# Optimization experiments

Hardware: AMD Instinct MI355X
Metric: run time of the kernel (lower is better)

## Reference

```python
import jax, jax.numpy as jnp
import numpy as np

CHUNK = 32
H = 4

def silu(x):
    return x * jax.nn.sigmoid(x)

def l2norm(x):
    return x * jax.lax.rsqrt(jnp.sum(x * x, -1, keepdims=True) + 1e-6)

def dwconv_causal(x_cl, w):
    # x_cl: (b, C, L), w: (C, k) depthwise causal conv (cross-correlation, left pad k-1)
    k = w.shape[1]
    xp = jnp.pad(x_cl, ((0, 0), (0, 0), (k - 1, 0)))
    return jax.lax.conv_general_dilated(xp, w[:, None, :], (1,), 'VALID',
        dimension_numbers=('NCH', 'OIH', 'NCH'), feature_group_count=x_cl.shape[1])

def short_conv_silu(x_bld, w):
    y = dwconv_causal(jnp.swapaxes(x_bld, 1, 2), w)
    return silu(jnp.swapaxes(y, 1, 2))

def delta_rule_chunkwise(q, k, v, beta, chunk=CHUNK):
    # q,k: (b,h,L,dk)  v: (b,h,L,dv)  beta: (b,h,L)
    b, h, L, dk = q.shape
    dv = v.shape[-1]
    pad = (-L) % chunk
    if pad:
        q, k, v = (jnp.pad(t, ((0, 0), (0, 0), (0, pad), (0, 0))) for t in (q, k, v))
        beta = jnp.pad(beta, ((0, 0), (0, 0), (0, pad)))
    n = (L + pad) // chunk
    q = l2norm(q)
    k = l2norm(k)
    v = v * beta[..., None]
    kb = k * beta[..., None]
    ch = lambda x: x.reshape(b, h, n, chunk, x.shape[-1])
    qc, kc, vc, kbc = map(ch, (q, k, v, kb))
    idx = jnp.arange(chunk)
    strict_lower = (idx[:, None] > idx[None, :]).astype(q.dtype)
    incl_lower = (idx[:, None] >= idx[None, :]).astype(q.dtype)
    # forward substitution to invert (I - tril(beta K K^T, -1)) per chunk
    attn = -jnp.einsum('bhncd,bhned->bhnce', kbc, kc) * strict_lower
    for i in range(1, chunk):
        upd = jnp.einsum('...j,...ji->...i', attn[..., i, :], attn[..., :, :i])
        attn = attn.at[..., i, :i].add(upd)
    attn = attn + jnp.eye(chunk, dtype=q.dtype)
    u = attn @ vc          # (b,h,n,c,dv)
    w = attn @ kbc         # (b,h,n,c,dk)
    xs = tuple(jnp.moveaxis(t, 2, 0) for t in (qc, kc, u, w))
    S0 = jnp.zeros((b, h, dk, dv), q.dtype)
    def step(S, x):
        qi, ki, ui, wi = x
        a_loc = jnp.einsum('bhcd,bhed->bhce', qi, ki) * incl_lower
        ui = ui - wi @ S
        oi = qi @ S + a_loc @ ui
        S = S + jnp.einsum('bhcd,bhcv->bhdv', ki, ui)
        return S, oi
    S, o = jax.lax.scan(step, S0, xs)
    o = jnp.moveaxis(o, 0, 2).reshape(b, h, n * chunk, dv)[:, :, :L]
    return o, S

def multiscale_conv(v, ms_w3, ms_w15, ms_w31, kernel_mix_w, channel_mixer_w):
    # v: (b,l,h,d)
    b, l, h, d = v.shape
    x = jnp.swapaxes(v.reshape(b, l, h * d), 1, 2)  # (b, h*d, l)
    outs = [dwconv_causal(x, w) for w in (ms_w3, ms_w15, ms_w31)]
    y = jnp.concatenate(outs, axis=1)               # (b, 3*h*d, l)
    # faithful to torch rearrange 'b (h kd) l -> b l h kd' on the concat layout
    y = y.reshape(b, h, 3 * d, l).transpose(0, 3, 1, 2)  # (b,l,h,3d)
    y = y @ kernel_mix_w                            # (b,l,h,d)
    y = (y.reshape(b, l, h * d) @ channel_mixer_w).reshape(b, l, h, d)
    return y

def _forward(hidden_states, Wq, Wk, Wv, Wb, conv_q_w, conv_k_w, conv_v_w,
             ms_w3, ms_w15, ms_w31, kernel_mix_w, channel_mixer_w,
             fusion_w1, fusion_b1, fusion_w2, fusion_b2, o_norm_w, Wo):
    b, L, D = hidden_states.shape
    h = H
    dk = Wq.shape[1] // h
    dv = Wv.shape[1] // h
    q = short_conv_silu(hidden_states @ Wq, conv_q_w).reshape(b, L, h, dk)
    k = short_conv_silu(hidden_states @ Wk, conv_k_w).reshape(b, L, h, dk)
    v = short_conv_silu(hidden_states @ Wv, conv_v_w).reshape(b, L, h, dv)
    v_direct = v
    beta = jax.nn.sigmoid(hidden_states @ Wb)  # (b,L,h)
    tr = lambda x: jnp.swapaxes(x, 1, 2)
    delta_out, _S = delta_rule_chunkwise(tr(q), tr(k), tr(v), tr(beta))
    delta_out = jnp.swapaxes(delta_out, 1, 2)  # (b,L,h,dv)
    ms_out = multiscale_conv(v_direct, ms_w3, ms_w15, ms_w31, kernel_mix_w, channel_mixer_w)
    bn = lambda x: jnp.mean(jnp.abs(x), -1)    # (b,L,h)
    gate_features = jnp.concatenate([hidden_states, bn(ms_out), bn(delta_out), bn(v_direct)], -1)
    hdn = jax.nn.gelu(gate_features @ fusion_w1 + fusion_b1, approximate=False)
    logits = (hdn @ fusion_w2 + fusion_b2).reshape(b, L, h, 3)
    wts = jax.nn.softmax(logits, -1)
    o = wts[..., 0:1] * ms_out + wts[..., 1:2] * delta_out + wts[..., 2:3] * v_direct
    o = o * jax.lax.rsqrt(jnp.mean(o * o, -1, keepdims=True) + 1e-5) * o_norm_w  # RMSNorm
    return o.reshape(b, L, h * dv) @ Wo

def setup_inputs() -> dict:
    B, L, D = 4, 2048, 1024
    h, d = H, D // H
    key = jax.random.key(0)
    ks = jax.random.split(key, 20)
    nrm = lambda k, shp, s: (jax.random.normal(k, shp, dtype=jnp.float32) * s)
    inp = {
        'hidden_states': nrm(ks[0], (B, L, D), 1.0),
        'Wq': nrm(ks[1], (D, D), D ** -0.5),
        'Wk': nrm(ks[2], (D, D), D ** -0.5),
        'Wv': nrm(ks[3], (D, D), D ** -0.5),
        'Wb': nrm(ks[4], (D, h), D ** -0.5),
        'conv_q_w': nrm(ks[5], (D, 4), 0.3),
        'conv_k_w': nrm(ks[6], (D, 4), 0.3),
        'conv_v_w': nrm(ks[7], (D, 4), 0.3),
        'ms_w3': nrm(ks[8], (D, 3), 0.02),
        'ms_w15': nrm(ks[9], (D, 15), 0.02),
        'ms_w31': nrm(ks[10], (D, 31), 0.02),
        'kernel_mix_w': nrm(ks[11], (3 * d, d), (3 * d) ** -0.5),
        'channel_mixer_w': nrm(ks[12], (D, D), D ** -0.5),
        'fusion_w1': nrm(ks[13], (D + 3 * h, 2 * D), (D + 3 * h) ** -0.5),
        'fusion_b1': jnp.zeros((2 * D,), jnp.float32),
        'fusion_w2': nrm(ks[14], (2 * D, 3 * h), (2 * D) ** -0.5),
        'fusion_b2': jnp.concatenate([jnp.zeros((2 * h,), jnp.float32), jnp.ones((h,), jnp.float32)]),
        'o_norm_w': jnp.ones((d,), jnp.float32),
        'Wo': nrm(ks[15], (D, D), D ** -0.5),
    }
    return inp

def reference(hidden_states, Wq, Wk, Wv, Wb, conv_q_w, conv_k_w, conv_v_w,
              ms_w3, ms_w15, ms_w31, kernel_mix_w, channel_mixer_w,
              fusion_w1, fusion_b1, fusion_w2, fusion_b2, o_norm_w, Wo):
    return _forward(hidden_states, Wq, Wk, Wv, Wb, conv_q_w, conv_k_w, conv_v_w,
                    ms_w3, ms_w15, ms_w31, kernel_mix_w, channel_mixer_w,
                    fusion_w1, fusion_b1, fusion_w2, fusion_b2, o_norm_w, Wo)
```

## Files before the change

kernel.cpp:

```cpp
#include <hip/hip_runtime.h>
#include <math.h>


typedef __attribute__((ext_vector_type(8))) __bf16 bf16x8;
typedef __attribute__((ext_vector_type(4))) float f32x4;

__device__ inline ushort f2bf(float f) {
    union { float f; unsigned u; } x; x.f = f;
    unsigned u = x.u;
    u += 0x7fffu + ((u >> 16) & 1u);
    return (ushort)(u >> 16);
}
__device__ inline float bf2f(ushort h) {
    union { unsigned u; float f; } x; x.u = ((unsigned)h) << 16;
    return x.f;
}
__device__ inline float ldf(float v) { return v; }
__device__ inline float ldf(ushort v) { return bf2f(v); }

template<int EPI>
__global__ __launch_bounds__(256) void gemm_mfma(
    const ushort* __restrict__ A, const ushort* __restrict__ BT,
    const float* __restrict__ bias, const float* __restrict__ extA,
    const float* __restrict__ extB, void* __restrict__ Cout,
    int M, int N, int K)
{
    __shared__ ushort As[128 * 32];
    __shared__ ushort Bs[128 * 32];
    __shared__ float bns[(EPI >= 2) ? 128 * 13 : 1];
    __shared__ float exb[(EPI >= 2) ? 12 * 128 : 1];
    const int tid = threadIdx.x;
    const int row0 = blockIdx.y * 128, col0 = blockIdx.x * 128;
    const int lane = tid & 63, wave = tid >> 6;
    const int wr = (wave >> 1) * 64, wc = (wave & 1) * 64;

    if (EPI >= 2) {
        for (int e = tid; e < 128 * 12; e += 256)
            bns[(e / 12) * 13 + (e % 12)] = extA[(long)(row0 + e / 12) * 12 + e % 12];
        for (int e = tid; e < 12 * 128; e += 256)
            exb[e] = extB[(long)(e >> 7) * N + col0 + (e & 127)];
    }

    f32x4 acc[4][4];
    #pragma unroll
    for (int m = 0; m < 4; ++m)
        #pragma unroll
        for (int n = 0; n < 4; ++n) {
            acc[m][n][0] = 0.f; acc[m][n][1] = 0.f;
            acc[m][n][2] = 0.f; acc[m][n][3] = 0.f;
        }

    const int rA = lane & 15;
    const int ko = (lane >> 4) * 8;
    const int srow = tid >> 2;
    const int skk = (tid & 3) * 8;

    for (int k0 = 0; k0 < K; k0 += 32) {
        #pragma unroll
        for (int i = 0; i < 2; ++i) {
            const long ga = (long)(row0 + i * 64 + srow) * K + k0 + skk;
            __builtin_amdgcn_global_load_lds(
                (const __attribute__((address_space(1))) void*)(A + ga),
                (__attribute__((address_space(3))) void*)(As + i * 2048 + wave * 512),
                16, 0, 0);
            const long gb = (long)(col0 + i * 64 + srow) * K + k0 + skk;
            __builtin_amdgcn_global_load_lds(
                (const __attribute__((address_space(1))) void*)(BT + gb),
                (__attribute__((address_space(3))) void*)(Bs + i * 2048 + wave * 512),
                16, 0, 0);
        }
        __syncthreads();
        bf16x8 af[4], bfr[4];
        #pragma unroll
        for (int m = 0; m < 4; ++m)
            af[m] = *(const bf16x8*)(As + (wr + m * 16 + rA) * 32 + ko);
        #pragma unroll
        for (int n = 0; n < 4; ++n)
            bfr[n] = *(const bf16x8*)(Bs + (wc + n * 16 + rA) * 32 + ko);
        #pragma unroll
        for (int m = 0; m < 4; ++m)
            #pragma unroll
            for (int n = 0; n < 4; ++n)
                acc[m][n] = __builtin_amdgcn_mfma_f32_16x16x32_bf16(af[m], bfr[n], acc[m][n], 0, 0, 0);
        __syncthreads();
    }

    const int crow = (lane >> 4) * 4;
    const int ccol = lane & 15;
    #pragma unroll
    for (int m = 0; m < 4; ++m) {
        #pragma unroll
        for (int n = 0; n < 4; ++n) {
            #pragma unroll
            for (int r = 0; r < 4; ++r) {
                const int rl = wr + m * 16 + crow + r;
                const int cl = wc + n * 16 + ccol;
                float vv = acc[m][n][r];
                if (EPI >= 2) {
                    vv += bias[col0 + cl];
                    #pragma unroll
                    for (int j = 0; j < 12; ++j) vv += bns[rl * 13 + j] * exb[j * 128 + cl];
                    vv = 0.5f * vv * (1.f + erff(vv * 0.70710678118654752f));
                }
                const long off = (long)(row0 + rl) * N + col0 + cl;
                if (EPI == 0) ((float*)Cout)[off] = vv;
                else ((ushort*)Cout)[off] = f2bf(vv);
            }
        }
    }
}

__global__ __launch_bounds__(256) void transpose_cast(const float* __restrict__ W,
    ushort* __restrict__ WT, int K, int N)
{
    __shared__ float t[32][33];
    const int k0 = blockIdx.y * 32, n0 = blockIdx.x * 32;
    const int c = threadIdx.x & 31, r8 = threadIdx.x >> 5;
    #pragma unroll
    for (int rr = 0; rr < 4; ++rr) {
        const int r = r8 + rr * 8;
        t[r][c] = W[(long)(k0 + r) * N + n0 + c];
    }
    __syncthreads();
    #pragma unroll
    for (int rr = 0; rr < 4; ++rr) {
        const int r = r8 + rr * 8;
        WT[(long)(n0 + r) * K + k0 + c] = f2bf(t[c][r]);
    }
}

__global__ __launch_bounds__(256) void cast_bf16(const float* __restrict__ x,
    ushort* __restrict__ y)
{
    const long i = ((long)blockIdx.x * 256 + threadIdx.x) * 4;
    const float4 v = *(const float4*)(x + i);
    ushort4 o;
    o.x = f2bf(v.x); o.y = f2bf(v.y); o.z = f2bf(v.z); o.w = f2bf(v.w);
    *(ushort4*)(y + i) = o;
}

template<int NOUT, int MODE, typename TA>
__global__ __launch_bounds__(256) void gemm_smallN(const TA* __restrict__ A,
    const float* __restrict__ Bm, const float* __restrict__ bias,
    float* __restrict__ Cm, int K)
{
    __shared__ float part[4][NOUT];
    __shared__ float sm[NOUT];
    const int m = blockIdx.x, tid = threadIdx.x;
    const TA* ar = A + (long)m * K;
    float acc[NOUT];
    #pragma unroll
    for (int j = 0; j < NOUT; ++j) acc[j] = 0.f;
    for (int k = tid; k < K; k += 256) {
        const float a = ldf(ar[k]);
        #pragma unroll
        for (int j = 0; j < NOUT; ++j) acc[j] += a * Bm[(long)k * NOUT + j];
    }
    #pragma unroll
    for (int j = 0; j < NOUT; ++j)
        for (int off = 32; off > 0; off >>= 1) acc[j] += __shfl_down(acc[j], off);
    const int wid = tid >> 6, lane = tid & 63;
    if (lane == 0) {
        #pragma unroll
        for (int j = 0; j < NOUT; ++j) part[wid][j] = acc[j];
    }
    __syncthreads();
    if (tid < NOUT) {
        float s = part[0][tid] + part[1][tid] + part[2][tid] + part[3][tid];
        if (MODE == 0) {
            Cm[(long)m * NOUT + tid] = 1.f / (1.f + expf(-s));
        } else {
            sm[tid] = s + bias[tid];
        }
    }
    if (MODE == 1) {
        __syncthreads();
        if (tid < NOUT) {
            const int hh = tid / 3, r = tid - hh * 3;
            const float a0 = sm[hh * 3], a1 = sm[hh * 3 + 1], a2 = sm[hh * 3 + 2];
            const float mx = fmaxf(a0, fmaxf(a1, a2));
            const float e0 = expf(a0 - mx), e1 = expf(a1 - mx), e2 = expf(a2 - mx);
            const float mine = (r == 0) ? e0 : ((r == 1) ? e1 : e2);
            Cm[(long)m * NOUT + tid] = mine / (e0 + e1 + e2);
        }
    }
}

__global__ __launch_bounds__(256) void conv4_silu(const float* __restrict__ x,
    const float* __restrict__ wc, float* __restrict__ y)
{
    const long idx = (long)blockIdx.x * 256 + threadIdx.x;
    const int c = (int)(idx & 1023);
    const long bl = idx >> 10;
    const int l = (int)(bl & 2047);
    const long b = bl >> 11;
    const float* xp = x + b * 2048 * 1024 + c;
    const float* wp = wc + c * 4;
    float s = 0.f;
    #pragma unroll
    for (int t = 0; t < 4; ++t) {
        const int ll = l - 3 + t;
        if (ll >= 0) s += xp[(long)ll * 1024] * wp[t];
    }
    y[idx] = s / (1.f + expf(-s));
}

__global__ __launch_bounds__(256) void l2norm_bf16(const float* __restrict__ x,
    ushort* __restrict__ y)
{
    const long wid = ((long)blockIdx.x * 256 + threadIdx.x) >> 6;
    const int lane = threadIdx.x & 63;
    const float4 xv = *(const float4*)(x + wid * 256 + lane * 4);
    float ss = xv.x * xv.x + xv.y * xv.y + xv.z * xv.z + xv.w * xv.w;
    for (int off = 32; off > 0; off >>= 1) ss += __shfl_down(ss, off);
    ss = __shfl(ss, 0);
    const float inv = rsqrtf(ss + 1e-6f);
    ushort4 o;
    o.x = f2bf(xv.x * inv); o.y = f2bf(xv.y * inv);
    o.z = f2bf(xv.z * inv); o.w = f2bf(xv.w * inv);
    *(ushort4*)(y + wid * 256 + lane * 4) = o;
}

__global__ __launch_bounds__(256) void chunk_prep(
    const ushort* __restrict__ qn, const ushort* __restrict__ kn,
    const float* __restrict__ v, const float* __restrict__ beta,
    float* __restrict__ u, ushort* __restrict__ w16,
    ushort* __restrict__ kT16, ushort* __restrict__ al16)
{
    __shared__ float kb_s[32 * 256];
    __shared__ float bufB[32 * 256];
    __shared__ float Ms[32 * 33];
    __shared__ float Rs[32 * 33];
    __shared__ float bet[32];
    const int blk = blockIdx.x;
    const int n = blk & 63;
    const int bh = blk >> 6;
    const int h = bh & 3;
    const int b = bh >> 2;
    const int tid = threadIdx.x;
    const long lbase = (long)b * 2048 + n * 32;

    if (tid < 32) bet[tid] = beta[(lbase + tid) * 4 + h];
    __syncthreads();
    for (int e = tid; e < 8192; e += 256) {
        const int c = e >> 8, dd = e & 255;
        const float kv = bf2f(kn[(lbase + c) * 1024 + h * 256 + dd]);
        bufB[dd * 32 + c] = kv;
        kb_s[c * 256 + dd] = kv * bet[c];
    }
    __syncthreads();
    for (int e = tid; e < 8192; e += 256)
        kT16[(long)blk * 8192 + e] = f2bf(bufB[e]);

    const int j = tid & 31, i0 = tid >> 5;
    {
        float m4[4] = {0.f, 0.f, 0.f, 0.f};
        for (int dd = 0; dd < 256; ++dd) {
            const float kt = bufB[dd * 32 + j];
            #pragma unroll
            for (int ii = 0; ii < 4; ++ii) m4[ii] += kb_s[(i0 + 8 * ii) * 256 + dd] * kt;
        }
        #pragma unroll
        for (int ii = 0; ii < 4; ++ii) {
            const int i = i0 + 8 * ii;
            const float mv = (i > j) ? -m4[ii] : 0.f;
            Ms[i * 33 + j] = mv;
            Rs[i * 33 + j] = mv + ((i == j) ? 1.f : 0.f);
        }
    }
    {
        float a4[4] = {0.f, 0.f, 0.f, 0.f};
        for (int dd = 0; dd < 256; ++dd) {
            const float kt = bufB[dd * 32 + j];
            #pragma unroll
            for (int ii = 0; ii < 4; ++ii)
                a4[ii] += bf2f(qn[(lbase + (i0 + 8 * ii)) * 1024 + h * 256 + dd]) * kt;
        }
        #pragma unroll
        for (int ii = 0; ii < 4; ++ii) {
            const int i = i0 + 8 * ii;
            al16[(long)blk * 1024 + i * 32 + j] = f2bf((i >= j) ? a4[ii] : 0.f);
        }
    }
    __syncthreads();
    for (int it = 0; it < 4; ++it) {
        float p4[4] = {0.f, 0.f, 0.f, 0.f};
        for (int kk = 0; kk < 32; ++kk) {
            const float pb = Ms[kk * 33 + j];
            #pragma unroll
            for (int ii = 0; ii < 4; ++ii) p4[ii] += Ms[(i0 + 8 * ii) * 33 + kk] * pb;
        }
        __syncthreads();
        #pragma unroll
        for (int ii = 0; ii < 4; ++ii) Ms[(i0 + 8 * ii) * 33 + j] = p4[ii];
        __syncthreads();
        float r4[4] = {0.f, 0.f, 0.f, 0.f};
        for (int kk = 0; kk < 32; ++kk) {
            const float pb = Ms[kk * 33 + j];
            #pragma unroll
            for (int ii = 0; ii < 4; ++ii) r4[ii] += Rs[(i0 + 8 * ii) * 33 + kk] * pb;
        }
        __syncthreads();
        #pragma unroll
        for (int ii = 0; ii < 4; ++ii) Rs[(i0 + 8 * ii) * 33 + j] += r4[ii];
        __syncthreads();
    }
    for (int e = tid; e < 8192; e += 256) {
        const int c = e >> 8, dd = e & 255;
        bufB[c * 256 + dd] = v[(lbase + c) * 1024 + h * 256 + dd] * bet[c];
    }
    __syncthreads();
    {
        const int dd = tid;
        float accU[32], accW[32];
        #pragma unroll
        for (int r = 0; r < 32; ++r) { accU[r] = 0.f; accW[r] = 0.f; }
        for (int kk = 0; kk < 32; ++kk) {
            const float vv = bufB[kk * 256 + dd];
            const float bb = kb_s[kk * 256 + dd];
            #pragma unroll
            for (int r = 0; r < 32; ++r) {
                const float rr = Rs[r * 33 + kk];
                accU[r] += rr * vv;
                accW[r] += rr * bb;
            }
        }
        const long base = (long)blk * 32;
        #pragma unroll
        for (int r = 0; r < 32; ++r) {
            u  [(base + r) * 256 + dd] = accU[r];
            w16[(base + r) * 256 + dd] = f2bf(accW[r]);
        }
    }
}

__global__ __launch_bounds__(64) void delta_scan_mfma(
    const ushort* __restrict__ q16, const ushort* __restrict__ kT16,
    const ushort* __restrict__ w16, const float* __restrict__ u,
    const ushort* __restrict__ al16, float* __restrict__ dt)
{
    __shared__ __align__(16) ushort Stg[2][25600];
    __shared__ __align__(16) ushort Sb[16 * 264];
    __shared__ __align__(16) ushort Ub[16 * 40];
    const int blk = blockIdx.x;
    const int bh = blk & 15;
    const int sl = blk >> 4;
    const int h = bh & 3;
    const int b = bh >> 2;
    const int v0 = sl * 16;
    const int lane = threadIdx.x;
    const int col = lane & 15;
    const int grp = lane >> 4;
    const int l5 = lane & 31;
    const int lh = lane >> 5;

    f32x4 S[16];
    #pragma unroll
    for (int t = 0; t < 16; ++t) { S[t][0] = 0.f; S[t][1] = 0.f; S[t][2] = 0.f; S[t][3] = 0.f; }
    for (int i = lane; i < 16 * 264; i += 64) Sb[i] = 0;

    const ushort* Wg = w16  + (long)bh * 64 * 8192;
    const ushort* Qg = q16  + ((long)b * 2048) * 1024 + h * 256;
    const ushort* Kg = kT16 + (long)bh * 64 * 8192;
    const ushort* Ag = al16 + (long)bh * 64 * 1024;
    const float*  Ug = u    + (long)bh * 64 * 8192 + grp * 1024 + v0 + col;
    float*        dp = dt   + ((long)b * 2048 + grp * 4) * 1024 + h * 256 + v0 + col;

    auto STAGE = [&](int n, int s) {
        ushort* dst = &Stg[s][0];
        const ushort* wsrc = Wg + (long)n * 8192;
        #pragma unroll
        for (int i = 0; i < 16; ++i) {
            const int row = 2 * i + lh;
            const int key = row & 7;
            __builtin_amdgcn_global_load_lds(
                (const __attribute__((address_space(1))) void*)(wsrc + row * 256 + ((l5 ^ key) << 3)),
                (__attribute__((address_space(3))) void*)(dst + i * 512), 16, 0, 0);
        }
        #pragma unroll
        for (int i = 0; i < 16; ++i) {
            const int row = 2 * i + lh;
            const int key = row & 7;
            __builtin_amdgcn_global_load_lds(
                (const __attribute__((address_space(1))) void*)(Qg + (long)(n * 32 + row) * 1024 + ((l5 ^ key) << 3)),
                (__attribute__((address_space(3))) void*)(dst + 8192 + i * 512), 16, 0, 0);
        }
        const ushort* ksrc = Kg + (long)n * 8192;
        #pragma unroll
        for (int i = 0; i < 16; ++i)
            __builtin_amdgcn_global_load_lds(
                (const __attribute__((address_space(1))) void*)(ksrc + i * 512 + lane * 8),
                (__attribute__((address_space(3))) void*)(dst + 16384 + i * 512), 16, 0, 0);
        const ushort* asrc = Ag + (long)n * 1024;
        #pragma unroll
        for (int i = 0; i < 2; ++i)
            __builtin_amdgcn_global_load_lds(
                (const __attribute__((address_space(1))) void*)(asrc + i * 512 + lane * 8),
                (__attribute__((address_space(3))) void*)(dst + 24576 + i * 512), 16, 0, 0);
    };

    const int xk = (col & 7) << 3;

    STAGE(0, 0);
    for (int n = 0; n < 64; ++n) {
        const int s = n & 1;
        asm volatile("s_waitcnt vmcnt(0)" ::: "memory");
        __builtin_amdgcn_sched_barrier(0);
        float upre[8];
        #pragma unroll
        for (int rt = 0; rt < 2; ++rt)
            #pragma unroll
            for (int r = 0; r < 4; ++r)
                upre[rt * 4 + r] = Ug[(long)n * 8192 + rt * 4096 + r * 256];
        __builtin_amdgcn_sched_barrier(0);
        if (n < 63) STAGE(n + 1, s ^ 1);
        const ushort* Sg = &Stg[s][0];

        bf16x8 sf[8];
        #pragma unroll
        for (int kb = 0; kb < 8; ++kb)
            sf[kb] = *(const bf16x8*)&Sb[col * 264 + kb * 32 + grp * 8];

        f32x4 up[2];
        #pragma unroll
        for (int rt = 0; rt < 2; ++rt) {
            f32x4 a; a[0] = 0.f; a[1] = 0.f; a[2] = 0.f; a[3] = 0.f;
            #pragma unroll
            for (int kb = 0; kb < 8; ++kb) {
                const int widx = ((rt * 16 + col) << 8) + (((kb << 5) + (grp << 3)) ^ xk);
                const bf16x8 wf = *(const bf16x8*)&Sg[widx];
                a = __builtin_amdgcn_mfma_f32_16x16x32_bf16(wf, sf[kb], a, 0, 0, 0);
            }
            #pragma unroll
            for (int r = 0; r < 4; ++r)
                up[rt][r] = upre[rt * 4 + r] - a[r];
        }
        #pragma unroll
        for (int rt = 0; rt < 2; ++rt) {
            ushort4 p;
            p.x = f2bf(up[rt][0]); p.y = f2bf(up[rt][1]);
            p.z = f2bf(up[rt][2]); p.w = f2bf(up[rt][3]);
            *(ushort4*)&Ub[col * 40 + rt * 16 + grp * 4] = p;
        }
        const bf16x8 uf = *(const bf16x8*)&Ub[col * 40 + grp * 8];

        #pragma unroll
        for (int rt = 0; rt < 2; ++rt) {
            f32x4 a; a[0] = 0.f; a[1] = 0.f; a[2] = 0.f; a[3] = 0.f;
            #pragma unroll
            for (int kb = 0; kb < 8; ++kb) {
                const int qidx = 8192 + ((rt * 16 + col) << 8) + (((kb << 5) + (grp << 3)) ^ xk);
                const bf16x8 qf = *(const bf16x8*)&Sg[qidx];
                a = __builtin_amdgcn_mfma_f32_16x16x32_bf16(qf, sf[kb], a, 0, 0, 0);
            }
            const bf16x8 alf = *(const bf16x8*)&Sg[24576 + rt * 512 + col * 32 + grp * 8];
            a = __builtin_amdgcn_mfma_f32_16x16x32_bf16(alf, uf, a, 0, 0, 0);
            #pragma unroll
            for (int r = 0; r < 4; ++r)
                dp[(long)n * 32768 + rt * 16384 + r * 1024] = a[r];
        }

        #pragma unroll
        for (int t = 0; t < 16; ++t) {
            const bf16x8 kf = *(const bf16x8*)&Sg[16384 + t * 512 + col * 32 + grp * 8];
            S[t] = __builtin_amdgcn_mfma_f32_16x16x32_bf16(kf, uf, S[t], 0, 0, 0);
        }

        #pragma unroll
        for (int t = 0; t < 16; ++t) {
            ushort4 p;
            p.x = f2bf(S[t][0]); p.y = f2bf(S[t][1]);
            p.z = f2bf(S[t][2]); p.w = f2bf(S[t][3]);
            *(ushort4*)&Sb[col * 264 + t * 16 + grp * 4] = p;
        }
    }
}

__global__ __launch_bounds__(256) void ms_conv(const float* __restrict__ v,
    const float* __restrict__ w3, const float* __restrict__ w15,
    const float* __restrict__ w31, ushort* __restrict__ y)
{
    const int bid = blockIdx.x;
    const int b = bid >> 10;
    const int oct = (bid >> 2) & 255;
    const int c = ((bid & 3) << 8) + threadIdx.x;
    const int l0 = oct << 3;
    const float* vb = v + ((long)b * 2048) * 1024 + c;
    ushort* yb = y + ((long)b * 2048) * 3072 + c;

    float win[38];
    #pragma unroll
    for (int t = 0; t < 38; ++t) {
        const int ll = l0 - 30 + t;
        win[t] = (ll >= 0) ? vb[(long)ll * 1024] : 0.f;
    }
    {
        float W[31];
        #pragma unroll
        for (int t = 0; t < 31; ++t) W[t] = w31[c * 31 + t];
        #pragma unroll
        for (int j = 0; j < 8; ++j) {
            float s = 0.f;
            #pragma unroll
            for (int t = 0; t < 31; ++t) s += win[j + t] * W[t];
            yb[(long)(l0 + j) * 3072 + 2048] = f2bf(s);
        }
    }
    {
        float W[15];
        #pragma unroll
        for (int t = 0; t < 15; ++t) W[t] = w15[c * 15 + t];
        #pragma unroll
        for (int j = 0; j < 8; ++j) {
            float s = 0.f;
            #pragma unroll
            for (int t = 0; t < 15; ++t) s += win[j + 16 + t] * W[t];
            yb[(long)(l0 + j) * 3072 + 1024] = f2bf(s);
        }
    }
    {
        float W[3];
        #pragma unroll
        for (int t = 0; t < 3; ++t) W[t] = w3[c * 3 + t];
        #pragma unroll
        for (int j = 0; j < 8; ++j) {
            float s = 0.f;
            #pragma unroll
            for (int t = 0; t < 3; ++t) s += win[j + 28 + t] * W[t];
            yb[(long)(l0 + j) * 3072] = f2bf(s);
        }
    }
}

__global__ __launch_bounds__(256) void build_bn(const float* __restrict__ ms,
    const float* __restrict__ dt, const float* __restrict__ v,
    float* __restrict__ bn)
{
    const int bl = blockIdx.x, tid = threadIdx.x;
    const long rb = (long)bl * 1024;
    const int wid = tid >> 6, lane = tid & 63;
    const long base = rb + wid * 256 + lane * 4;
    float* g = bn + (long)bl * 12;
    float4 a;
    float s;
    a = *(const float4*)(ms + base);
    s = fabsf(a.x) + fabsf(a.y) + fabsf(a.z) + fabsf(a.w);
    for (int off = 32; off > 0; off >>= 1) s += __shfl_down(s, off);
    if (lane == 0) g[wid] = s * (1.f / 256.f);
    a = *(const float4*)(dt + base);
    s = fabsf(a.x) + fabsf(a.y) + fabsf(a.z) + fabsf(a.w);
    for (int off = 32; off > 0; off >>= 1) s += __shfl_down(s, off);
    if (lane == 0) g[4 + wid] = s * (1.f / 256.f);
    a = *(const float4*)(v + base);
    s = fabsf(a.x) + fabsf(a.y) + fabsf(a.z) + fabsf(a.w);
    for (int off = 32; off > 0; off >>= 1) s += __shfl_down(s, off);
    if (lane == 0) g[8 + wid] = s * (1.f / 256.f);
}

__global__ __launch_bounds__(256) void blend_rms(const float* __restrict__ ms,
    const float* __restrict__ dt, const float* __restrict__ v,
    const float* __restrict__ wts, const float* __restrict__ onw,
    ushort* __restrict__ o)
{
    const int bl = blockIdx.x, tid = threadIdx.x;
    const int wid = tid >> 6, lane = tid & 63;
    const long base = (long)bl * 1024 + wid * 256 + lane * 4;
    const float* wr = wts + (long)bl * 12 + wid * 3;
    const float w0 = wr[0], w1 = wr[1], w2 = wr[2];
    const float4 m = *(const float4*)(ms + base);
    const float4 d = *(const float4*)(dt + base);
    const float4 x = *(const float4*)(v + base);
    float4 ov;
    ov.x = w0 * m.x + w1 * d.x + w2 * x.x;
    ov.y = w0 * m.y + w1 * d.y + w2 * x.y;
    ov.z = w0 * m.z + w1 * d.z + w2 * x.z;
    ov.w = w0 * m.w + w1 * d.w + w2 * x.w;
    float ss = ov.x * ov.x + ov.y * ov.y + ov.z * ov.z + ov.w * ov.w;
    for (int off = 32; off > 0; off >>= 1) ss += __shfl_down(ss, off);
    ss = __shfl(ss, 0);
    const float inv = rsqrtf(ss * (1.f / 256.f) + 1e-5f);
    const float4 nw = *(const float4*)(onw + lane * 4);
    ushort4 ob;
    ob.x = f2bf(ov.x * inv * nw.x); ob.y = f2bf(ov.y * inv * nw.y);
    ob.z = f2bf(ov.z * inv * nw.z); ob.w = f2bf(ov.w * inv * nw.w);
    *(ushort4*)(o + base) = ob;
}

extern "C" void kernel_launch(void* const* d_in, const int* in_sizes, int n_in,
                              void* d_out, int out_size, void* d_ws, size_t ws_size,
                              hipStream_t stream)
{
    (void)in_sizes; (void)n_in; (void)out_size; (void)ws_size;
    const float* hid   = (const float*)d_in[0];
    const float* Wq    = (const float*)d_in[1];
    const float* Wk    = (const float*)d_in[2];
    const float* Wv    = (const float*)d_in[3];
    const float* Wb    = (const float*)d_in[4];
    const float* cq    = (const float*)d_in[5];
    const float* ck    = (const float*)d_in[6];
    const float* cv    = (const float*)d_in[7];
    const float* w3    = (const float*)d_in[8];
    const float* w15   = (const float*)d_in[9];
    const float* w31   = (const float*)d_in[10];
    const float* kmix  = (const float*)d_in[11];
    const float* cmix  = (const float*)d_in[12];
    const float* fw1   = (const float*)d_in[13];
    const float* fb1   = (const float*)d_in[14];
    const float* fw2   = (const float*)d_in[15];
    const float* fb2   = (const float*)d_in[16];
    const float* onw   = (const float*)d_in[17];
    const float* Wo    = (const float*)d_in[18];
    float* out = (float*)d_out;

    const size_t MiB = 1024 * 1024;
    char* W = (char*)d_ws;
    float*  s0    = (float*)(W);
    char*   s1c   = W + 32 * MiB;
    float*  s1    = (float*)s1c;
    float*  s2    = (float*)(W + 64 * MiB);
    char*   s3    = W + 96 * MiB;
    float*  s4    = (float*)(W + 128 * MiB);
    ushort* hid16 = (ushort*)(W + 160 * MiB);
    ushort* WqT   = (ushort*)(W + 176 * MiB);
    ushort* WkT   = WqT   + 1024 * 1024;
    ushort* WvT   = WkT   + 1024 * 1024;
    ushort* cmixT = WvT   + 1024 * 1024;
    ushort* WoT   = cmixT + 1024 * 1024;
    ushort* fw1T  = WoT   + 1024 * 1024;
    ushort* kmixT = fw1T  + 2048 * 1024;
    float*  beta  = (float*)(W + 191 * MiB);
    ushort* al16  = (ushort*)(W + 191 * MiB + 128 * 1024);
    float*  bnf   = (float*)(W + 193 * MiB + 128 * 1024);
    float*  wts   = bnf + 98304;

    ushort* q16    = (ushort*)s3;
    ushort* k16    = (ushort*)(s3 + 16 * MiB);
    ushort* mix16  = q16;
    ushort* ofin16 = k16;
    ushort* yms16  = (ushort*)s0;
    ushort* hdn16  = (ushort*)s0;
    float*  qlin = s0; float* qtmp = s1;
    float*  u = s0;
    ushort* w16  = (ushort*)s1c;
    ushort* kT16 = (ushort*)(s1c + 16 * MiB);
    float*  dt = s2; float* v = s4; float* msout = s1;

    const dim3 T256(256);
    cast_bf16<<<8192, T256, 0, stream>>>(hid, hid16);
    transpose_cast<<<dim3(32, 32), T256, 0, stream>>>(Wq, WqT, 1024, 1024);
    transpose_cast<<<dim3(32, 32), T256, 0, stream>>>(Wk, WkT, 1024, 1024);
    transpose_cast<<<dim3(32, 32), T256, 0, stream>>>(Wv, WvT, 1024, 1024);
    transpose_cast<<<dim3(32, 32), T256, 0, stream>>>(cmix, cmixT, 1024, 1024);
    transpose_cast<<<dim3(32, 32), T256, 0, stream>>>(Wo, WoT, 1024, 1024);
    transpose_cast<<<dim3(64, 32), T256, 0, stream>>>(fw1, fw1T, 1024, 2048);
    transpose_cast<<<dim3(8, 24), T256, 0, stream>>>(kmix, kmixT, 768, 256);
    gemm_mfma<0><<<dim3(8, 64), T256, 0, stream>>>(hid16, WqT, nullptr, nullptr, nullptr, qlin, 8192, 1024, 1024);
    conv4_silu<<<32768, T256, 0, stream>>>(qlin, cq, qtmp);
    l2norm_bf16<<<8192, T256, 0, stream>>>(qtmp, q16);
    gemm_mfma<0><<<dim3(8, 64), T256, 0, stream>>>(hid16, WkT, nullptr, nullptr, nullptr, qlin, 8192, 1024, 1024);
    conv4_silu<<<32768, T256, 0, stream>>>(qlin, ck, qtmp);
    l2norm_bf16<<<8192, T256, 0, stream>>>(qtmp, k16);
    gemm_mfma<0><<<dim3(8, 64), T256, 0, stream>>>(hid16, WvT, nullptr, nullptr, nullptr, qlin, 8192, 1024, 1024);
    conv4_silu<<<32768, T256, 0, stream>>>(qlin, cv, v);
    gemm_smallN<4, 0><<<8192, T256, 0, stream>>>(hid, Wb, nullptr, beta, 1024);
    chunk_prep<<<1024, T256, 0, stream>>>(q16, k16, v, beta, u, w16, kT16, al16);
    delta_scan_mfma<<<256, dim3(64), 0, stream>>>(q16, kT16, w16, u, al16, dt);
    ms_conv<<<4096, T256, 0, stream>>>(v, w3, w15, w31, yms16);
    gemm_mfma<1><<<dim3(2, 256), T256, 0, stream>>>(yms16, kmixT, nullptr, nullptr, nullptr, mix16, 32768, 256, 768);
    gemm_mfma<0><<<dim3(8, 64), T256, 0, stream>>>(mix16, cmixT, nullptr, nullptr, nullptr, msout, 8192, 1024, 1024);
    build_bn<<<8192, T256, 0, stream>>>(msout, dt, v, bnf);
    gemm_mfma<3><<<dim3(16, 64), T256, 0, stream>>>(hid16, fw1T, fb1, bnf, fw1 + 1024L * 2048, hdn16, 8192, 2048, 1024);
    gemm_smallN<12, 1><<<8192, T256, 0, stream>>>(hdn16, fw2, fb2, wts, 2048);
    blend_rms<<<8192, T256, 0, stream>>>(msout, dt, v, wts, onw, ofin16);
    gemm_mfma<0><<<dim3(8, 64), T256, 0, stream>>>(ofin16, WoT, nullptr, nullptr, nullptr, out, 8192, 1024, 1024);
}
```

Before: 875.9 us.

## Share staged W/K/alpha tiles across four waves in the delta scan

```diff
diff --git a/kernel.cpp b/kernel.cpp
--- a/kernel.cpp
+++ b/kernel.cpp
@@ -334,21 +334,24 @@
     }
 }
 
-__global__ __launch_bounds__(64) void delta_scan_mfma(
+__global__ __launch_bounds__(256) void delta_scan_mfma(
     const ushort* __restrict__ q16, const ushort* __restrict__ kT16,
     const ushort* __restrict__ w16, const float* __restrict__ u,
     const ushort* __restrict__ al16, float* __restrict__ dt)
 {
-    __shared__ __align__(16) ushort Stg[2][25600];
-    __shared__ __align__(16) ushort Sb[16 * 264];
-    __shared__ __align__(16) ushort Ub[16 * 40];
+    __shared__ __align__(16) ushort Stg[2][17408];
+    __shared__ __align__(16) ushort Sb[4][16 * 264];
+    __shared__ __align__(16) ushort Ub[4][16 * 40];
     const int blk = blockIdx.x;
     const int bh = blk & 15;
-    const int sl = blk >> 4;
+    const int qtr = blk >> 4;
+    const int tid = threadIdx.x;
+    const int wv = tid >> 6;
+    const int lane = tid & 63;
+    const int sl = qtr * 4 + wv;
     const int h = bh & 3;
     const int b = bh >> 2;
     const int v0 = sl * 16;
-    const int lane = threadIdx.x;
     const int col = lane & 15;
     const int grp = lane >> 4;
     const int l5 = lane & 31;
@@ -357,46 +360,44 @@
     f32x4 S[16];
     #pragma unroll
     for (int t = 0; t < 16; ++t) { S[t][0] = 0.f; S[t][1] = 0.f; S[t][2] = 0.f; S[t][3] = 0.f; }
-    for (int i = lane; i < 16 * 264; i += 64) Sb[i] = 0;
+    for (int i = lane; i < 16 * 264; i += 64) Sb[wv][i] = 0;
 
     const ushort* Wg = w16  + (long)bh * 64 * 8192;
     const ushort* Qg = q16  + ((long)b * 2048) * 1024 + h * 256;
     const ushort* Kg = kT16 + (long)bh * 64 * 8192;
     const ushort* Ag = al16 + (long)bh * 64 * 1024;
     const float*  Ug = u    + (long)bh * 64 * 8192 + grp * 1024 + v0 + col;
+    const ushort* qp = Qg + col * 1024 + grp * 8;
     float*        dp = dt   + ((long)b * 2048 + grp * 4) * 1024 + h * 256 + v0 + col;
 
-    auto STAGE = [&](int n, int s) {
-        ushort* dst = &Stg[s][0];
+    auto STAGE = [&](int n, int sb) {
+        ushort* dst = &Stg[sb][0];
         const ushort* wsrc = Wg + (long)n * 8192;
         #pragma unroll
-        for (int i = 0; i < 16; ++i) {
-            const int row = 2 * i + lh;
+        for (int i = 0; i < 4; ++i) {
+            const int blkW = wv * 4 + i;
+            const int row = 2 * blkW + lh;
             const int key = row & 7;
             __builtin_amdgcn_global_load_lds(
                 (const __attribute__((address_space(1))) void*)(wsrc + row * 256 + ((l5 ^ key) << 3)),
-                (__attribute__((address_space(3))) void*)(dst + i * 512), 16, 0, 0);
-        }
-        #pragma unroll
-        for (int i = 0; i < 16; ++i) {
-            const int row = 2 * i + lh;
-            const int key = row & 7;
+                (__attribute__((address_space(3))) void*)(dst + blkW * 512), 16, 0, 0);
+        }
+        const ushort* ksrc = Kg + (long)n * 8192;
+        #pragma unroll
+        for (int i = 0; i < 4; ++i) {
+            const int j = wv * 4 + i;
             __builtin_amdgcn_global_load_lds(
-                (const __attribute__((address_space(1))) void*)(Qg + (long)(n * 32 + row) * 1024 + ((l5 ^ key) << 3)),
-                (__attribute__((address_space(3))) void*)(dst + 8192 + i * 512), 16, 0, 0);
-        }
-        const ushort* ksrc = Kg + (long)n * 8192;
-        #pragma unroll
-        for (int i = 0; i < 16; ++i)
-            __builtin_amdgcn_global_load_lds(
-                (const __attribute__((address_space(1))) void*)(ksrc + i * 512 + lane * 8),
-                (__attribute__((address_space(3))) void*)(dst + 16384 + i * 512), 16, 0, 0);
-        const ushort* asrc = Ag + (long)n * 1024;
-        #pragma unroll
-        for (int i = 0; i < 2; ++i)
-            __builtin_amdgcn_global_load_lds(
-                (const __attribute__((address_space(1))) void*)(asrc + i * 512 + lane * 8),
-                (__attribute__((address_space(3))) void*)(dst + 24576 + i * 512), 16, 0, 0);
+                (const __attribute__((address_space(1))) void*)(ksrc + j * 512 + lane * 8),
+                (__attribute__((address_space(3))) void*)(dst + 8192 + j * 512), 16, 0, 0);
+        }
+        if (wv == 0) {
+            const ushort* asrc = Ag + (long)n * 1024;
+            #pragma unroll
+            for (int i = 0; i < 2; ++i)
+                __builtin_amdgcn_global_load_lds(
+                    (const __attribute__((address_space(1))) void*)(asrc + i * 512 + lane * 8),
+                    (__attribute__((address_space(3))) void*)(dst + 16384 + i * 512), 16, 0, 0);
+        }
     };
 
     const int xk = (col & 7) << 3;
@@ -404,22 +405,39 @@
     STAGE(0, 0);
     for (int n = 0; n < 64; ++n) {
         const int s = n & 1;
-        asm volatile("s_waitcnt vmcnt(0)" ::: "memory");
         __builtin_amdgcn_sched_barrier(0);
+        __builtin_amdgcn_s_barrier();
+        __builtin_amdgcn_sched_barrier(0);
+        if (n < 63) {
+            STAGE(n + 1, s ^ 1);
+            if (wv == 0) asm volatile("s_waitcnt vmcnt(10)" ::: "memory");
+            else         asm volatile("s_waitcnt vmcnt(8)"  ::: "memory");
+        } else {
+            asm volatile("s_waitcnt vmcnt(0)" ::: "memory");
+        }
+        __builtin_amdgcn_sched_barrier(0);
+        __builtin_amdgcn_s_barrier();
+        __builtin_amdgcn_sched_barrier(0);
+        const ushort* Sg = &Stg[s][0];
+
         float upre[8];
         #pragma unroll
         for (int rt = 0; rt < 2; ++rt)
             #pragma unroll
             for (int r = 0; r < 4; ++r)
                 upre[rt * 4 + r] = Ug[(long)n * 8192 + rt * 4096 + r * 256];
-        __builtin_amdgcn_sched_barrier(0);
-        if (n < 63) STAGE(n + 1, s ^ 1);
-        const ushort* Sg = &Stg[s][0];
 
         bf16x8 sf[8];
         #pragma unroll
         for (int kb = 0; kb < 8; ++kb)
-            sf[kb] = *(const bf16x8*)&Sb[col * 264 + kb * 32 + grp * 8];
+            sf[kb] = *(const bf16x8*)&Sb[wv][col * 264 + kb * 32 + grp * 8];
+
+        bf16x8 qf[2][8];
+        #pragma unroll
+        for (int rt = 0; rt < 2; ++rt)
+            #pragma unroll
+            for (int kb = 0; kb < 8; ++kb)
+                qf[rt][kb] = *(const bf16x8*)(qp + (long)n * 32768 + rt * 16384 + kb * 32);
 
         f32x4 up[2];
         #pragma unroll
@@ -440,20 +458,17 @@
             ushort4 p;
             p.x = f2bf(up[rt][0]); p.y = f2bf(up[rt][1]);
             p.z = f2bf(up[rt][2]); p.w = f2bf(up[rt][3]);
-            *(ushort4*)&Ub[col * 40 + rt * 16 + grp * 4] = p;
-        }
-        const bf16x8 uf = *(const bf16x8*)&Ub[col * 40 + grp * 8];
+            *(ushort4*)&Ub[wv][col * 40 + rt * 16 + grp * 4] = p;
+        }
+        const bf16x8 uf = *(const bf16x8*)&Ub[wv][col * 40 + grp * 8];
 
         #pragma unroll
         for (int rt = 0; rt < 2; ++rt) {
             f32x4 a; a[0] = 0.f; a[1] = 0.f; a[2] = 0.f; a[3] = 0.f;
             #pragma unroll
-            for (int kb = 0; kb < 8; ++kb) {
-                const int qidx = 8192 + ((rt * 16 + col) << 8) + (((kb << 5) + (grp << 3)) ^ xk);
-                const bf16x8 qf = *(const bf16x8*)&Sg[qidx];
-                a = __builtin_amdgcn_mfma_f32_16x16x32_bf16(qf, sf[kb], a, 0, 0, 0);
-            }
-            const bf16x8 alf = *(const bf16x8*)&Sg[24576 + rt * 512 + col * 32 + grp * 8];
+            for (int kb = 0; kb < 8; ++kb)
+                a = __builtin_amdgcn_mfma_f32_16x16x32_bf16(qf[rt][kb], sf[kb], a, 0, 0, 0);
+            const bf16x8 alf = *(const bf16x8*)&Sg[16384 + rt * 512 + col * 32 + grp * 8];
             a = __builtin_amdgcn_mfma_f32_16x16x32_bf16(alf, uf, a, 0, 0, 0);
             #pragma unroll
             for (int r = 0; r < 4; ++r)
@@ -462,7 +477,7 @@
 
         #pragma unroll
         for (int t = 0; t < 16; ++t) {
-            const bf16x8 kf = *(const bf16x8*)&Sg[16384 + t * 512 + col * 32 + grp * 8];
+            const bf16x8 kf = *(const bf16x8*)&Sg[8192 + t * 512 + col * 32 + grp * 8];
             S[t] = __builtin_amdgcn_mfma_f32_16x16x32_bf16(kf, uf, S[t], 0, 0, 0);
         }
 
@@ -471,7 +486,7 @@
             ushort4 p;
             p.x = f2bf(S[t][0]); p.y = f2bf(S[t][1]);
             p.z = f2bf(S[t][2]); p.w = f2bf(S[t][3]);
-            *(ushort4*)&Sb[col * 264 + t * 16 + grp * 4] = p;
+            *(ushort4*)&Sb[wv][col * 264 + t * 16 + grp * 4] = p;
         }
     }
 }
@@ -664,7 +679,7 @@
     conv4_silu<<<32768, T256, 0, stream>>>(qlin, cv, v);
     gemm_smallN<4, 0><<<8192, T256, 0, stream>>>(hid, Wb, nullptr, beta, 1024);
     chunk_prep<<<1024, T256, 0, stream>>>(q16, k16, v, beta, u, w16, kT16, al16);
-    delta_scan_mfma<<<256, dim3(64), 0, stream>>>(q16, kT16, w16, u, al16, dt);
+    delta_scan_mfma<<<64, T256, 0, stream>>>(q16, kT16, w16, u, al16, dt);
     ms_conv<<<4096, T256, 0, stream>>>(v, w3, w15, w31, yms16);
     gemm_mfma<1><<<dim3(2, 256), T256, 0, stream>>>(yms16, kmixT, nullptr, nullptr, nullptr, mix16, 32768, 256, 768);
     gemm_mfma<0><<<dim3(8, 64), T256, 0, stream>>>(mix16, cmixT, nullptr, nullptr, nullptr, msout, 8192, 1024, 1024);
```

After: 936.4 us. 1.07x slower.
